# Kernel optimization log

Hardware: AMD Instinct MI355X
Metric: run time of the kernel (lower is better)

## Reference

```python
import jax, jax.numpy as jnp
import numpy as np

N = 50000        # nodes
E = 1600000      # edges (before self loops)
IN = 256         # in_channels
C = 32           # hidden_channels (per head)
H = 4            # heads
OUT = 64         # out_channels
NEG_SLOPE = 0.2  # PyG GATConv default


def setup_inputs() -> dict:
    key = jax.random.key(0)
    ks = jax.random.split(key, 8)
    x = jax.random.normal(ks[0], (N, IN), dtype=jnp.float32)
    edge_index = jax.random.randint(ks[1], (2, E), 0, N, dtype=jnp.int64)
    s = 0.05
    W = jax.random.normal(ks[2], (IN, H * C), dtype=jnp.float32) * s
    att_src = jax.random.normal(ks[3], (H, C), dtype=jnp.float32) * s
    att_dst = jax.random.normal(ks[4], (H, C), dtype=jnp.float32) * s
    bias = jnp.zeros((H * C,), dtype=jnp.float32)
    lin_W = jax.random.normal(ks[5], (H * C, OUT), dtype=jnp.float32) * s
    lin_b = jnp.zeros((OUT,), dtype=jnp.float32)
    return {"x": x, "edge_index": edge_index, "W": W, "att_src": att_src,
            "att_dst": att_dst, "bias": bias, "lin_W": lin_W, "lin_b": lin_b}


def reference(x, edge_index, W, att_src, att_dst, bias, lin_W, lin_b):
    # Linear transform per head: [N, H, C]
    h = (x @ W).reshape(N, H, C)
    # Per-node attention halves (PyG GATConv): [N, H]
    a_src = jnp.einsum('nhc,hc->nh', h, att_src)
    a_dst = jnp.einsum('nhc,hc->nh', h, att_dst)
    # Add self loops (PyG default add_self_loops=True)
    loop = jnp.arange(N, dtype=edge_index.dtype)
    src = jnp.concatenate([edge_index[0], loop])  # message source j
    dst = jnp.concatenate([edge_index[1], loop])  # message target i
    # Edge attention logits: LeakyReLU(a_src[j] + a_dst[i])  -> [E+N, H]
    e = jax.nn.leaky_relu(a_src[src] + a_dst[dst], negative_slope=NEG_SLOPE)
    # Segment softmax over incoming edges of each destination node
    emax = jax.lax.stop_gradient(jax.ops.segment_max(e, dst, num_segments=N))
    emax = jnp.where(jnp.isfinite(emax), emax, 0.0)
    ex = jnp.exp(e - emax[dst])
    denom = jax.ops.segment_sum(ex, dst, num_segments=N)
    alpha = ex / denom[dst]  # [E+N, H]; self loops guarantee denom > 0
    # Weighted scatter-sum of source features: [N, H, C]
    msg = alpha[:, :, None] * h[src]
    agg = jax.ops.segment_sum(msg, dst, num_segments=N)
    out = agg.reshape(N, H * C) + bias  # concat heads + bias
    out = jax.nn.elu(out)
    return out @ lin_W + lin_b
```

## Files before the change

### kernel.cpp

```cpp
#include <hip/hip_runtime.h>
#include <cstdint>
#include <cstddef>

#define N_NODES 50000
#define N_EDGES 1600000
#define TOT_E   (N_EDGES + N_NODES)
#define IN_DIM  256
#define HC      128
#define NHEAD   4
#define OUT_DIM 64

#define SHIFT   7
#define BSZ     128
#define NBUK    ((N_NODES + BSZ - 1) / BSZ)
#define CHUNK   2048
#define EPT     8
#define NCHUNK  ((TOT_E + CHUNK - 1) / CHUNK)
#define NREP    8
#define CAPR    768
#define CAP     (NREP * CAPR)
#define STRIDE  88
#define ROWW    (STRIDE / 2)

#define K1_ROWS 32
#define XPAD 264
#define HPAD 132
#define K1_NB ((N_NODES + K1_ROWS - 1) / K1_ROWS)

#define W2_GEMM_BLK ((HC * IN_DIM) / 256)
#define W2_LIN_BLK  ((OUT_DIM * HC) / 256)

typedef __attribute__((ext_vector_type(8))) short bf16x8;
typedef __attribute__((ext_vector_type(4))) float f32x4;
typedef __attribute__((ext_vector_type(4))) unsigned short u16x4;

static __device__ __forceinline__ uint16_t f2bf(float f) {
    uint32_t u = __float_as_uint(f);
    uint32_t r = (u + 0x7fffu + ((u >> 16) & 1u)) >> 16;
    return (uint16_t)r;
}
static __device__ __forceinline__ float bf_lo(uint32_t u) {
    return __uint_as_float(u << 16);
}
static __device__ __forceinline__ float bf_hi(uint32_t u) {
    return __uint_as_float(u & 0xffff0000u);
}

__global__ __launch_bounds__(256) void w2bf(const float* __restrict__ W,
                                            const float* __restrict__ linW,
                                            uint16_t* __restrict__ wt,
                                            uint16_t* __restrict__ lwt,
                                            int* __restrict__ gcur) {
    if (blockIdx.x < W2_GEMM_BLK) {
        int idx = blockIdx.x * 256 + threadIdx.x;
        int n = idx >> 8, k = idx & 255;
        wt[idx] = f2bf(W[(size_t)k * HC + n]);
        if (idx < NBUK * NREP) gcur[idx] = 0;
    } else {
        int idx = (blockIdx.x - W2_GEMM_BLK) * 256 + threadIdx.x;
        int n = idx >> 7, k = idx & 127;
        float w = linW[(size_t)k * OUT_DIM + n];
        uint16_t h = f2bf(w);
        float hf = __uint_as_float((uint32_t)h << 16);
        lwt[idx] = h;
        lwt[OUT_DIM * HC + idx] = f2bf(w - hf);
    }
}

__global__ __launch_bounds__(256) void k1p3(const float* __restrict__ x,
                                            const uint16_t* __restrict__ wt,
                                            const float* __restrict__ att_src,
                                            const float* __restrict__ att_dst,
                                            uint16_t* __restrict__ hb,
                                            float* __restrict__ a_src,
                                            float* __restrict__ a_dst,
                                            const int* __restrict__ ei,
                                            int* __restrict__ gcur,
                                            uint32_t* __restrict__ binned) {
    __shared__ char smem[K1_ROWS * 528];
    __shared__ float att_s[HC], att_d[HC];
    const int tid = threadIdx.x;

    if (blockIdx.x < K1_NB) {
        uint16_t* xs = (uint16_t*)smem;
        float*    hs = (float*)smem;
        const int wave = tid >> 6;
        const int lane = tid & 63;
        const int m    = lane & 15;
        const int q    = lane >> 4;
        const int row0 = blockIdx.x * K1_ROWS;
        const int wr   = (wave >> 1) * 16;
        const int wc   = (wave & 1) * 64;

        if (tid < HC) { att_s[tid] = att_src[tid]; att_d[tid] = att_dst[tid]; }

        for (int i = tid * 4; i < K1_ROWS * IN_DIM; i += 1024) {
            int r = i >> 8, c = i & 255;
            int gr = row0 + r;
            float4 v = make_float4(0.f, 0.f, 0.f, 0.f);
            if (gr < N_NODES) v = *(const float4*)(x + (size_t)gr * IN_DIM + c);
            uint32_t lo = (uint32_t)f2bf(v.x) | ((uint32_t)f2bf(v.y) << 16);
            uint32_t hi = (uint32_t)f2bf(v.z) | ((uint32_t)f2bf(v.w) << 16);
            *(uint2*)(xs + r * XPAD + c) = make_uint2(lo, hi);
        }
        __syncthreads();

        f32x4 acc[4];
        #pragma unroll
        for (int t = 0; t < 4; ++t) acc[t] = (f32x4){0.f, 0.f, 0.f, 0.f};

        const int arow = wr + m;
        #pragma unroll
        for (int ks = 0; ks < IN_DIM; ks += 32) {
            bf16x8 a = *(const bf16x8*)(xs + arow * XPAD + ks + q * 8);
            #pragma unroll
            for (int t = 0; t < 4; ++t) {
                bf16x8 b = *(const bf16x8*)(wt + (size_t)(wc + t * 16 + m) * IN_DIM + ks + q * 8);
                acc[t] = __builtin_amdgcn_mfma_f32_16x16x32_bf16(a, b, acc[t], 0, 0, 0);
            }
        }
        __syncthreads();

        #pragma unroll
        for (int t = 0; t < 4; ++t)
            #pragma unroll
            for (int r = 0; r < 4; ++r)
                hs[(wr + q * 4 + r) * HPAD + wc + t * 16 + m] = acc[t][r];
        __syncthreads();

        for (int i = tid * 4; i < K1_ROWS * HC; i += 1024) {
            int r = i >> 7, c = i & 127;
            if (row0 + r < N_NODES) {
                float4 v = *(const float4*)(hs + r * HPAD + c);
                uint32_t lo = (uint32_t)f2bf(v.x) | ((uint32_t)f2bf(v.y) << 16);
                uint32_t hi = (uint32_t)f2bf(v.z) | ((uint32_t)f2bf(v.w) << 16);
                *(uint2*)(hb + (size_t)(row0 + r) * HC + c) = make_uint2(lo, hi);
            }
        }
        if (tid < K1_ROWS * NHEAD) {
            int r = tid >> 2, hd = tid & 3;
            if (row0 + r < N_NODES) {
                float s = 0.f, d = 0.f;
                #pragma unroll
                for (int j = 0; j < 32; ++j) {
                    float v = hs[r * HPAD + hd * 32 + j];
                    s = fmaf(v, att_s[hd * 32 + j], s);
                    d = fmaf(v, att_d[hd * 32 + j], d);
                }
                a_src[(row0 + r) * NHEAD + hd] = s;
                a_dst[(row0 + r) * NHEAD + hd] = d;
            }
        }
    } else {
        int* hist = (int*)smem;
        int* lcur = hist + NBUK;
        for (int i = tid; i < NBUK; i += 256) hist[i] = 0;
        __syncthreads();

        uint32_t wreg[EPT];
        const int pblk = blockIdx.x - K1_NB;
        const int rep  = pblk & (NREP - 1);
        const int base = pblk * CHUNK;
        #pragma unroll
        for (int k = 0; k < EPT; ++k) {
            int e = base + k * 256 + tid;
            uint32_t word = 0xFFFFFFFFu;
            if (e < TOT_E) {
                int src, dst;
                if (e < N_EDGES) { src = ei[e]; dst = ei[N_EDGES + e]; }
                else             { src = e - N_EDGES; dst = src; }
                int b = dst >> SHIFT;
                word = (uint32_t)src | ((uint32_t)(dst & (BSZ - 1)) << 16)
                     | ((uint32_t)b << 23);
                atomicAdd(&hist[b], 1);
            }
            wreg[k] = word;
        }
        __syncthreads();
        for (int i = tid; i < NBUK; i += 256) {
            int c = hist[i];
            lcur[i] = c ? atomicAdd(&gcur[rep * NBUK + i], c) : 0;
        }
        __syncthreads();
        #pragma unroll
        for (int k = 0; k < EPT; ++k) {
            uint32_t word = wreg[k];
            if (word != 0xFFFFFFFFu) {
                int b = (int)(word >> 23);
                int pos = atomicAdd(&lcur[b], 1);
                if (pos < CAPR)
                    binned[(size_t)b * CAP + rep * CAPR + pos] = word;
            }
        }
    }
}

__global__ __launch_bounds__(256) void rgrp(const uint32_t* __restrict__ binned,
                                            const int* __restrict__ gcur,
                                            uint16_t* __restrict__ csr,
                                            int* __restrict__ cnt) {
    __shared__ uint32_t lcsr32[BSZ * ROWW];
    __shared__ int ncnt[BSZ];
    const int b   = blockIdx.x;
    const int tid = threadIdx.x;

    for (int j = tid; j < BSZ * ROWW; j += 256) lcsr32[j] = 0;
    if (tid < BSZ) ncnt[tid] = 0;
    __syncthreads();

    uint16_t* lcsr16 = (uint16_t*)lcsr32;
    #pragma unroll
    for (int rep = 0; rep < NREP; ++rep) {
        int c = gcur[rep * NBUK + b];
        if (c > CAPR) c = CAPR;
        const uint32_t* bb = binned + (size_t)b * CAP + rep * CAPR;
        for (int i = tid; i < c; i += 256) {
            uint32_t w = bb[i];
            int dl  = (w >> 16) & (BSZ - 1);
            int pos = atomicAdd(&ncnt[dl], 1);
            if (pos < STRIDE) lcsr16[dl * STRIDE + pos] = (uint16_t)(w & 0xFFFFu);
        }
    }
    __syncthreads();

    const int node0 = b * BSZ;
    uint32_t* csr32 = (uint32_t*)csr;
    for (int j = tid; j < BSZ * ROWW; j += 256) {
        int r = j / ROWW, w = j - r * ROWW;
        int node = node0 + r;
        if (node < N_NODES)
            csr32[(size_t)node * ROWW + w] = lcsr32[j];
    }
    if (tid < BSZ && node0 + tid < N_NODES) cnt[node0 + tid] = ncnt[tid];
}

__global__ __launch_bounds__(512, 6) void q4k7(const uint16_t* __restrict__ csr,
                                               const int* __restrict__ cnt,
                                               const uint32_t* __restrict__ hb32,
                                               const float* __restrict__ a_src,
                                               const float* __restrict__ a_dst,
                                               const float* __restrict__ bias,
                                               const uint16_t* __restrict__ lwt,
                                               const float* __restrict__ linb,
                                               float* __restrict__ out) {
    __shared__ uint16_t as_[32][136];
    const int tid  = threadIdx.x;
    const int wave = tid >> 6;
    const int lane = tid & 63;
    const int g    = lane >> 4;
    const int sl   = lane & 15;
    const int head = sl >> 2;
    const int baseln = g << 4;
    const char*  hb8 = (const char*)hb32 + sl * 16;
    const float* ash = a_src + head;
    const float4 bA = *(const float4*)(bias + sl * 8);
    const float4 bB = *(const float4*)(bias + sl * 8 + 4);

    const int ln   = wave * 4 + g;
    const int node = blockIdx.x * 32 + ln;
    int myc = 0;
    if (node < N_NODES) myc = min(cnt[node], STRIDE);
    const uint16_t* crow = csr + (size_t)min(node, N_NODES - 1) * STRIDE;

    int m1   = max(myc, __shfl_xor(myc, 16, 64));
    int maxc = max(m1,  __shfl_xor(m1, 32, 64));
    const int nit = (maxc + 3) >> 2;
    const float ad = a_dst[min(node, N_NODES - 1) * NHEAD + head];

    uint2 svq = *(const uint2*)(crow + sl * 4);
    const int svlo = (int)svq.x, svhi = (int)svq.y;

    float l = 0.f;
    float acc[8];
    #pragma unroll
    for (int j = 0; j < 8; ++j) acc[j] = 0.f;

    uint4 ph0 = make_uint4(0, 0, 0, 0), ph1 = ph0, ph2 = ph0, ph3 = ph0;
    float pa0 = 0.f, pa1 = 0.f, pa2 = 0.f, pa3 = 0.f;
    if (nit > 0) {
        uint32_t lo = (uint32_t)__shfl(svlo, baseln, 64);
        uint32_t hi = (uint32_t)__shfl(svhi, baseln, 64);
        int s0 = (int)(lo & 0xFFFFu), s1 = (int)(lo >> 16);
        int s2 = (int)(hi & 0xFFFFu), s3 = (int)(hi >> 16);
        pa0 = ash[s0 * NHEAD];
        pa1 = ash[s1 * NHEAD];
        pa2 = ash[s2 * NHEAD];
        pa3 = ash[s3 * NHEAD];
        ph0 = *(const uint4*)(hb8 + ((uint32_t)s0 << 8));
        ph1 = *(const uint4*)(hb8 + ((uint32_t)s1 << 8));
        ph2 = *(const uint4*)(hb8 + ((uint32_t)s2 << 8));
        ph3 = *(const uint4*)(hb8 + ((uint32_t)s3 << 8));
    }

    for (int it = 0; it < nit; ++it) {
        const int i = it * 4;
        const uint4 h0 = ph0, h1 = ph1, h2 = ph2, h3 = ph3;
        const float as0 = pa0, as1 = pa1, as2 = pa2, as3 = pa3;
        if (it + 1 < nit) {
            int s0, s1, s2, s3;
            if (it + 1 < 16) {
                uint32_t lo = (uint32_t)__shfl(svlo, baseln + it + 1, 64);
                uint32_t hi = (uint32_t)__shfl(svhi, baseln + it + 1, 64);
                s0 = (int)(lo & 0xFFFFu); s1 = (int)(lo >> 16);
                s2 = (int)(hi & 0xFFFFu); s3 = (int)(hi >> 16);
            } else {
                u16x4 nv = *(const u16x4*)(crow + i + 4);
                s0 = nv[0]; s1 = nv[1]; s2 = nv[2]; s3 = nv[3];
            }
            pa0 = ash[s0 * NHEAD];
            pa1 = ash[s1 * NHEAD];
            pa2 = ash[s2 * NHEAD];
            pa3 = ash[s3 * NHEAD];
            ph0 = *(const uint4*)(hb8 + ((uint32_t)s0 << 8));
            ph1 = *(const uint4*)(hb8 + ((uint32_t)s1 << 8));
            ph2 = *(const uint4*)(hb8 + ((uint32_t)s2 << 8));
            ph3 = *(const uint4*)(hb8 + ((uint32_t)s3 << 8));
        }

        float e0 = as0 + ad, e1 = as1 + ad, e2 = as2 + ad, e3 = as3 + ad;
        e0 = fmaxf(e0, 0.2f * e0);
        e1 = fmaxf(e1, 0.2f * e1);
        e2 = fmaxf(e2, 0.2f * e2);
        e3 = fmaxf(e3, 0.2f * e3);
        float w0 = __expf(e0), w1 = __expf(e1);
        float w2 = __expf(e2), w3 = __expf(e3);
        w0 = (i + 0 < myc) ? w0 : 0.f;
        w1 = (i + 1 < myc) ? w1 : 0.f;
        w2 = (i + 2 < myc) ? w2 : 0.f;
        w3 = (i + 3 < myc) ? w3 : 0.f;
        l += (w0 + w1) + (w2 + w3);
        acc[0] = fmaf(w0, bf_lo(h0.x), acc[0]); acc[0] = fmaf(w1, bf_lo(h1.x), acc[0]);
        acc[0] = fmaf(w2, bf_lo(h2.x), acc[0]); acc[0] = fmaf(w3, bf_lo(h3.x), acc[0]);
        acc[1] = fmaf(w0, bf_hi(h0.x), acc[1]); acc[1] = fmaf(w1, bf_hi(h1.x), acc[1]);
        acc[1] = fmaf(w2, bf_hi(h2.x), acc[1]); acc[1] = fmaf(w3, bf_hi(h3.x), acc[1]);
        acc[2] = fmaf(w0, bf_lo(h0.y), acc[2]); acc[2] = fmaf(w1, bf_lo(h1.y), acc[2]);
        acc[2] = fmaf(w2, bf_lo(h2.y), acc[2]); acc[2] = fmaf(w3, bf_lo(h3.y), acc[2]);
        acc[3] = fmaf(w0, bf_hi(h0.y), acc[3]); acc[3] = fmaf(w1, bf_hi(h1.y), acc[3]);
        acc[3] = fmaf(w2, bf_hi(h2.y), acc[3]); acc[3] = fmaf(w3, bf_hi(h3.y), acc[3]);
        acc[4] = fmaf(w0, bf_lo(h0.z), acc[4]); acc[4] = fmaf(w1, bf_lo(h1.z), acc[4]);
        acc[4] = fmaf(w2, bf_lo(h2.z), acc[4]); acc[4] = fmaf(w3, bf_lo(h3.z), acc[4]);
        acc[5] = fmaf(w0, bf_hi(h0.z), acc[5]); acc[5] = fmaf(w1, bf_hi(h1.z), acc[5]);
        acc[5] = fmaf(w2, bf_hi(h2.z), acc[5]); acc[5] = fmaf(w3, bf_hi(h3.z), acc[5]);
        acc[6] = fmaf(w0, bf_lo(h0.w), acc[6]); acc[6] = fmaf(w1, bf_lo(h1.w), acc[6]);
        acc[6] = fmaf(w2, bf_lo(h2.w), acc[6]); acc[6] = fmaf(w3, bf_lo(h3.w), acc[6]);
        acc[7] = fmaf(w0, bf_hi(h0.w), acc[7]); acc[7] = fmaf(w1, bf_hi(h1.w), acc[7]);
        acc[7] = fmaf(w2, bf_hi(h2.w), acc[7]); acc[7] = fmaf(w3, bf_hi(h3.w), acc[7]);
    }

    uint4 pk = make_uint4(0, 0, 0, 0);
    if (node < N_NODES) {
        const float inv = 1.f / l;
        float o[8];
        o[0] = fmaf(acc[0], inv, bA.x); o[1] = fmaf(acc[1], inv, bA.y);
        o[2] = fmaf(acc[2], inv, bA.z); o[3] = fmaf(acc[3], inv, bA.w);
        o[4] = fmaf(acc[4], inv, bB.x); o[5] = fmaf(acc[5], inv, bB.y);
        o[6] = fmaf(acc[6], inv, bB.z); o[7] = fmaf(acc[7], inv, bB.w);
        #pragma unroll
        for (int j = 0; j < 8; ++j)
            o[j] = (o[j] > 0.f) ? o[j] : (__expf(o[j]) - 1.f);
        pk.x = (uint32_t)f2bf(o[0]) | ((uint32_t)f2bf(o[1]) << 16);
        pk.y = (uint32_t)f2bf(o[2]) | ((uint32_t)f2bf(o[3]) << 16);
        pk.z = (uint32_t)f2bf(o[4]) | ((uint32_t)f2bf(o[5]) << 16);
        pk.w = (uint32_t)f2bf(o[6]) | ((uint32_t)f2bf(o[7]) << 16);
    }
    *(uint4*)(&as_[ln][sl * 8]) = pk;
    __syncthreads();

    const int m   = lane & 15;
    const int q   = lane >> 4;
    const int wr  = (wave >> 2) * 16;
    const int wcl = (wave & 3) * 16;
    const uint16_t* lwlo = lwt + OUT_DIM * HC;

    f32x4 oacc = (f32x4){0.f, 0.f, 0.f, 0.f};
    const int arow = wr + m;
    #pragma unroll
    for (int ks = 0; ks < HC; ks += 32) {
        bf16x8 a = *(const bf16x8*)(&as_[arow][ks + q * 8]);
        bf16x8 bh = *(const bf16x8*)(lwt  + (size_t)(wcl + m) * HC + ks + q * 8);
        bf16x8 bl = *(const bf16x8*)(lwlo + (size_t)(wcl + m) * HC + ks + q * 8);
        oacc = __builtin_amdgcn_mfma_f32_16x16x32_bf16(a, bh, oacc, 0, 0, 0);
        oacc = __builtin_amdgcn_mfma_f32_16x16x32_bf16(a, bl, oacc, 0, 0, 0);
    }

    const int col  = wcl + m;
    const float lb = linb[col];
    const int grow = blockIdx.x * 32 + wr + q * 4;
    #pragma unroll
    for (int r = 0; r < 4; ++r)
        if (grow + r < N_NODES)
            out[(size_t)(grow + r) * OUT_DIM + col] = oacc[r] + lb;
}

extern "C" void kernel_launch(void* const* d_in, const int* in_sizes, int n_in,
                              void* d_out, int out_size, void* d_ws, size_t ws_size,
                              hipStream_t stream) {
    (void)in_sizes; (void)n_in; (void)out_size; (void)ws_size;
    const float* x       = (const float*)d_in[0];
    const int*   ei      = (const int*)d_in[1];
    const float* W       = (const float*)d_in[2];
    const float* att_src = (const float*)d_in[3];
    const float* att_dst = (const float*)d_in[4];
    const float* bias    = (const float*)d_in[5];
    const float* linW    = (const float*)d_in[6];
    const float* linb    = (const float*)d_in[7];
    float*       out     = (float*)d_out;

    char*  ws  = (char*)d_ws;
    size_t off = 0;
    auto alloc = [&](size_t bytes) -> void* {
        void* p = ws + off;
        off += (bytes + 255) & ~(size_t)255;
        return p;
    };
    uint16_t* hb     = (uint16_t*)alloc((size_t)N_NODES * HC * 2);
    uint16_t* wt     = (uint16_t*)alloc((size_t)HC * IN_DIM * 2);
    float*    a_src  = (float*)alloc((size_t)N_NODES * NHEAD * 4);
    float*    a_dst  = (float*)alloc((size_t)N_NODES * NHEAD * 4);
    int*      gcur   = (int*)alloc((size_t)NBUK * NREP * 4);
    uint32_t* binned = (uint32_t*)alloc((size_t)NBUK * CAP * 4);
    int*      cnt    = (int*)alloc((size_t)N_NODES * 4);
    uint16_t* csr    = (uint16_t*)alloc((size_t)N_NODES * STRIDE * 2);
    uint16_t* lwt    = (uint16_t*)alloc((size_t)2 * OUT_DIM * HC * 2);

    w2bf<<<W2_GEMM_BLK + W2_LIN_BLK, 256, 0, stream>>>(W, linW, wt, lwt, gcur);
    k1p3<<<K1_NB + NCHUNK, 256, 0, stream>>>(x, wt, att_src, att_dst,
                                             hb, a_src, a_dst,
                                             ei, gcur, binned);
    rgrp<<<NBUK, 256, 0, stream>>>(binned, gcur, csr, cnt);
    q4k7<<<(N_NODES + 31) / 32, 512, 0, stream>>>(csr, cnt, (const uint32_t*)hb,
                                                  a_src, a_dst, bias,
                                                  lwt, linb, out);
}
```

Before: 214.8 us.

## Merge all four kernels into one cooperative persistent kernel with grid syncs

Replaces the four separate launches (weight conversion, GEMM plus binning, regrouping, aggregation plus output linear) with one cooperative persistent kernel. The phases are separated by grid-wide syncs and each phase loops over work units with a grid stride. The goal is to remove launch gaps and kernel-boundary drains. Block size grows to 512 and GEMM tiles grow to 64 rows. In exchange, occupancy is capped at the cooperative limit, the larger shared-memory footprint may cut blocks per CU, and the grid barriers add their own cost. The hardcoded 256 CUs also assumes a particular device.

```diff
diff --git a/kernel.cpp b/kernel.cpp
--- a/kernel.cpp
+++ b/kernel.cpp
@@ -1,6 +1,9 @@
 #include <hip/hip_runtime.h>
+#include <hip/hip_cooperative_groups.h>
 #include <cstdint>
 #include <cstddef>
+
+namespace cg = cooperative_groups;
 
 #define N_NODES 50000
 #define N_EDGES 1600000
@@ -14,21 +17,20 @@
 #define BSZ     128
 #define NBUK    ((N_NODES + BSZ - 1) / BSZ)
 #define CHUNK   2048
-#define EPT     8
-#define NCHUNK  ((TOT_E + CHUNK - 1) / CHUNK)
+#define EPT4    4
 #define NREP    8
 #define CAPR    768
 #define CAP     (NREP * CAPR)
 #define STRIDE  88
 #define ROWW    (STRIDE / 2)
 
-#define K1_ROWS 32
 #define XPAD 264
 #define HPAD 132
-#define K1_NB ((N_NODES + K1_ROWS - 1) / K1_ROWS)
-
-#define W2_GEMM_BLK ((HC * IN_DIM) / 256)
-#define W2_LIN_BLK  ((OUT_DIM * HC) / 256)
+
+#define K1U   ((N_NODES + 63) / 64)
+#define P3U   ((TOT_E + CHUNK - 1) / CHUNK)
+#define P1U   (K1U + P3U)
+#define Q4U   ((N_NODES + 31) / 32)
 
 typedef __attribute__((ext_vector_type(8))) short bf16x8;
 typedef __attribute__((ext_vector_type(4))) float f32x4;
@@ -46,350 +48,337 @@
     return __uint_as_float(u & 0xffff0000u);
 }
 
-__global__ __launch_bounds__(256) void w2bf(const float* __restrict__ W,
-                                            const float* __restrict__ linW,
-                                            uint16_t* __restrict__ wt,
-                                            uint16_t* __restrict__ lwt,
-                                            int* __restrict__ gcur) {
-    if (blockIdx.x < W2_GEMM_BLK) {
-        int idx = blockIdx.x * 256 + threadIdx.x;
+__global__ __launch_bounds__(512) void mega(
+        const float* x, const int* ei, const float* W, const float* linW,
+        const float* att_src, const float* att_dst, const float* bias,
+        const float* linb, float* out,
+        uint16_t* wt, uint16_t* lwt, uint16_t* hb,
+        float* a_src, float* a_dst, int* gcur, uint32_t* binned,
+        int* cnt, uint16_t* csr) {
+    cg::grid_group gg = cg::this_grid();
+    __shared__ char smem[64 * 528];
+    __shared__ float att_s[HC], att_d[HC];
+    const int tid  = threadIdx.x;
+    const int gtid = blockIdx.x * 512 + tid;
+    const int gstr = gridDim.x * 512;
+
+    if (tid < HC) { att_s[tid] = att_src[tid]; att_d[tid] = att_dst[tid]; }
+
+    for (int idx = gtid; idx < HC * IN_DIM; idx += gstr) {
         int n = idx >> 8, k = idx & 255;
         wt[idx] = f2bf(W[(size_t)k * HC + n]);
-        if (idx < NBUK * NREP) gcur[idx] = 0;
-    } else {
-        int idx = (blockIdx.x - W2_GEMM_BLK) * 256 + threadIdx.x;
-        int n = idx >> 7, k = idx & 127;
+    }
+    for (int j = gtid; j < OUT_DIM * HC; j += gstr) {
+        int n = j >> 7, k = j & 127;
         float w = linW[(size_t)k * OUT_DIM + n];
         uint16_t h = f2bf(w);
-        float hf = __uint_as_float((uint32_t)h << 16);
-        lwt[idx] = h;
-        lwt[OUT_DIM * HC + idx] = f2bf(w - hf);
-    }
-}
-
-__global__ __launch_bounds__(256) void k1p3(const float* __restrict__ x,
-                                            const uint16_t* __restrict__ wt,
-                                            const float* __restrict__ att_src,
-                                            const float* __restrict__ att_dst,
-                                            uint16_t* __restrict__ hb,
-                                            float* __restrict__ a_src,
-                                            float* __restrict__ a_dst,
-                                            const int* __restrict__ ei,
-                                            int* __restrict__ gcur,
-                                            uint32_t* __restrict__ binned) {
-    __shared__ char smem[K1_ROWS * 528];
-    __shared__ float att_s[HC], att_d[HC];
-    const int tid = threadIdx.x;
-
-    if (blockIdx.x < K1_NB) {
-        uint16_t* xs = (uint16_t*)smem;
-        float*    hs = (float*)smem;
+        lwt[j] = h;
+        lwt[OUT_DIM * HC + j] = f2bf(w - __uint_as_float((uint32_t)h << 16));
+    }
+    for (int i = gtid; i < NBUK * NREP; i += gstr) gcur[i] = 0;
+    gg.sync();
+
+    for (int u = blockIdx.x; u < P1U; u += gridDim.x) {
+        if (u < K1U) {
+            uint16_t* xs = (uint16_t*)smem;
+            float*    hs = (float*)smem;
+            const int wave = tid >> 6;
+            const int lane = tid & 63;
+            const int m    = lane & 15;
+            const int q    = lane >> 4;
+            const int row0 = u * 64;
+            const int wr   = (wave >> 1) * 16;
+            const int wc   = (wave & 1) * 64;
+
+            for (int i = tid * 4; i < 64 * IN_DIM; i += 2048) {
+                int r = i >> 8, c = i & 255;
+                int gr = row0 + r;
+                float4 v = make_float4(0.f, 0.f, 0.f, 0.f);
+                if (gr < N_NODES) v = *(const float4*)(x + (size_t)gr * IN_DIM + c);
+                uint32_t lo = (uint32_t)f2bf(v.x) | ((uint32_t)f2bf(v.y) << 16);
+                uint32_t hi = (uint32_t)f2bf(v.z) | ((uint32_t)f2bf(v.w) << 16);
+                *(uint2*)(xs + r * XPAD + c) = make_uint2(lo, hi);
+            }
+            __syncthreads();
+
+            f32x4 acc[4];
+            #pragma unroll
+            for (int t = 0; t < 4; ++t) acc[t] = (f32x4){0.f, 0.f, 0.f, 0.f};
+            const int arow = wr + m;
+            #pragma unroll
+            for (int ks = 0; ks < IN_DIM; ks += 32) {
+                bf16x8 a = *(const bf16x8*)(xs + arow * XPAD + ks + q * 8);
+                #pragma unroll
+                for (int t = 0; t < 4; ++t) {
+                    bf16x8 b = *(const bf16x8*)(wt + (size_t)(wc + t * 16 + m) * IN_DIM + ks + q * 8);
+                    acc[t] = __builtin_amdgcn_mfma_f32_16x16x32_bf16(a, b, acc[t], 0, 0, 0);
+                }
+            }
+            __syncthreads();
+
+            #pragma unroll
+            for (int t = 0; t < 4; ++t)
+                #pragma unroll
+                for (int r = 0; r < 4; ++r)
+                    hs[(wr + q * 4 + r) * HPAD + wc + t * 16 + m] = acc[t][r];
+            __syncthreads();
+
+            for (int i = tid * 4; i < 64 * HC; i += 2048) {
+                int r = i >> 7, c = i & 127;
+                if (row0 + r < N_NODES) {
+                    float4 v = *(const float4*)(hs + r * HPAD + c);
+                    uint32_t lo = (uint32_t)f2bf(v.x) | ((uint32_t)f2bf(v.y) << 16);
+                    uint32_t hi = (uint32_t)f2bf(v.z) | ((uint32_t)f2bf(v.w) << 16);
+                    *(uint2*)(hb + (size_t)(row0 + r) * HC + c) = make_uint2(lo, hi);
+                }
+            }
+            if (tid < 64 * NHEAD) {
+                int r = tid >> 2, hd = tid & 3;
+                if (row0 + r < N_NODES) {
+                    float s = 0.f, d = 0.f;
+                    #pragma unroll
+                    for (int j = 0; j < 32; ++j) {
+                        float v = hs[r * HPAD + hd * 32 + j];
+                        s = fmaf(v, att_s[hd * 32 + j], s);
+                        d = fmaf(v, att_d[hd * 32 + j], d);
+                    }
+                    a_src[(row0 + r) * NHEAD + hd] = s;
+                    a_dst[(row0 + r) * NHEAD + hd] = d;
+                }
+            }
+        } else {
+            int* hist = (int*)smem;
+            int* lcur = hist + NBUK;
+            for (int i = tid; i < NBUK; i += 512) hist[i] = 0;
+            __syncthreads();
+
+            uint32_t wreg[EPT4];
+            const int pblk = u - K1U;
+            const int rep  = pblk & (NREP - 1);
+            const int base = pblk * CHUNK;
+            #pragma unroll
+            for (int k = 0; k < EPT4; ++k) {
+                int e = base + k * 512 + tid;
+                uint32_t word = 0xFFFFFFFFu;
+                if (e < TOT_E) {
+                    int src, dst;
+                    if (e < N_EDGES) { src = ei[e]; dst = ei[N_EDGES + e]; }
+                    else             { src = e - N_EDGES; dst = src; }
+                    int b = dst >> SHIFT;
+                    word = (uint32_t)src | ((uint32_t)(dst & (BSZ - 1)) << 16)
+                         | ((uint32_t)b << 23);
+                    atomicAdd(&hist[b], 1);
+                }
+                wreg[k] = word;
+            }
+            __syncthreads();
+            for (int i = tid; i < NBUK; i += 512) {
+                int c = hist[i];
+                lcur[i] = c ? atomicAdd(&gcur[rep * NBUK + i], c) : 0;
+            }
+            __syncthreads();
+            #pragma unroll
+            for (int k = 0; k < EPT4; ++k) {
+                uint32_t word = wreg[k];
+                if (word != 0xFFFFFFFFu) {
+                    int b = (int)(word >> 23);
+                    int pos = atomicAdd(&lcur[b], 1);
+                    if (pos < CAPR)
+                        binned[(size_t)b * CAP + rep * CAPR + pos] = word;
+                }
+            }
+        }
+        __syncthreads();
+    }
+    gg.sync();
+
+    {
+        uint32_t* lcsr32 = (uint32_t*)smem;
+        int*      ncnt   = (int*)(smem + BSZ * ROWW * 4);
+        uint16_t* lcsr16 = (uint16_t*)lcsr32;
+        uint32_t* csr32g = (uint32_t*)csr;
+        for (int u = blockIdx.x; u < NBUK; u += gridDim.x) {
+            for (int j = tid; j < BSZ * ROWW; j += 512) lcsr32[j] = 0;
+            if (tid < BSZ) ncnt[tid] = 0;
+            __syncthreads();
+
+            #pragma unroll
+            for (int rep = 0; rep < NREP; ++rep) {
+                int c = gcur[rep * NBUK + u];
+                if (c > CAPR) c = CAPR;
+                const uint32_t* bb = binned + (size_t)u * CAP + rep * CAPR;
+                for (int i = tid; i < c; i += 512) {
+                    uint32_t w = bb[i];
+                    int dl  = (w >> 16) & (BSZ - 1);
+                    int pos = atomicAdd(&ncnt[dl], 1);
+                    if (pos < STRIDE) lcsr16[dl * STRIDE + pos] = (uint16_t)(w & 0xFFFFu);
+                }
+            }
+            __syncthreads();
+
+            const int node0 = u * BSZ;
+            for (int j = tid; j < BSZ * ROWW; j += 512) {
+                int r = j / ROWW, w = j - r * ROWW;
+                if (node0 + r < N_NODES)
+                    csr32g[(size_t)(node0 + r) * ROWW + w] = lcsr32[j];
+            }
+            if (tid < BSZ && node0 + tid < N_NODES) cnt[node0 + tid] = ncnt[tid];
+            __syncthreads();
+        }
+    }
+    gg.sync();
+
+    {
+        uint16_t (*as_)[136] = (uint16_t (*)[136])smem;
         const int wave = tid >> 6;
         const int lane = tid & 63;
-        const int m    = lane & 15;
-        const int q    = lane >> 4;
-        const int row0 = blockIdx.x * K1_ROWS;
-        const int wr   = (wave >> 1) * 16;
-        const int wc   = (wave & 1) * 64;
-
-        if (tid < HC) { att_s[tid] = att_src[tid]; att_d[tid] = att_dst[tid]; }
-
-        for (int i = tid * 4; i < K1_ROWS * IN_DIM; i += 1024) {
-            int r = i >> 8, c = i & 255;
-            int gr = row0 + r;
-            float4 v = make_float4(0.f, 0.f, 0.f, 0.f);
-            if (gr < N_NODES) v = *(const float4*)(x + (size_t)gr * IN_DIM + c);
-            uint32_t lo = (uint32_t)f2bf(v.x) | ((uint32_t)f2bf(v.y) << 16);
-            uint32_t hi = (uint32_t)f2bf(v.z) | ((uint32_t)f2bf(v.w) << 16);
-            *(uint2*)(xs + r * XPAD + c) = make_uint2(lo, hi);
+        const int g    = lane >> 4;
+        const int sl   = lane & 15;
+        const int head = sl >> 2;
+        const int baseln = g << 4;
+        const char*  hb8 = (const char*)hb + sl * 16;
+        const float* ash = a_src + head;
+        const float4 bA = *(const float4*)(bias + sl * 8);
+        const float4 bB = *(const float4*)(bias + sl * 8 + 4);
+        const uint16_t* lwlo = lwt + OUT_DIM * HC;
+
+        for (int u = blockIdx.x; u < Q4U; u += gridDim.x) {
+            const int ln   = wave * 4 + g;
+            const int node = u * 32 + ln;
+            int myc = 0;
+            if (node < N_NODES) myc = min(cnt[node], STRIDE);
+            const uint16_t* crow = csr + (size_t)min(node, N_NODES - 1) * STRIDE;
+
+            int m1   = max(myc, __shfl_xor(myc, 16, 64));
+            int maxc = max(m1,  __shfl_xor(m1, 32, 64));
+            const int nit = (maxc + 3) >> 2;
+            const float ad = a_dst[min(node, N_NODES - 1) * NHEAD + head];
+
+            uint2 svq = *(const uint2*)(crow + sl * 4);
+            const int svlo = (int)svq.x, svhi = (int)svq.y;
+
+            float l = 0.f;
+            float acc[8];
+            #pragma unroll
+            for (int j = 0; j < 8; ++j) acc[j] = 0.f;
+
+            uint4 ph0 = make_uint4(0, 0, 0, 0), ph1 = ph0, ph2 = ph0, ph3 = ph0;
+            float pa0 = 0.f, pa1 = 0.f, pa2 = 0.f, pa3 = 0.f;
+            if (nit > 0) {
+                uint32_t lo = (uint32_t)__shfl(svlo, baseln, 64);
+                uint32_t hi = (uint32_t)__shfl(svhi, baseln, 64);
+                int s0 = (int)(lo & 0xFFFFu), s1 = (int)(lo >> 16);
+                int s2 = (int)(hi & 0xFFFFu), s3 = (int)(hi >> 16);
+                pa0 = ash[s0 * NHEAD];
+                pa1 = ash[s1 * NHEAD];
+                pa2 = ash[s2 * NHEAD];
+                pa3 = ash[s3 * NHEAD];
+                ph0 = *(const uint4*)(hb8 + ((uint32_t)s0 << 8));
+                ph1 = *(const uint4*)(hb8 + ((uint32_t)s1 << 8));
+                ph2 = *(const uint4*)(hb8 + ((uint32_t)s2 << 8));
+                ph3 = *(const uint4*)(hb8 + ((uint32_t)s3 << 8));
+            }
+
+            for (int it = 0; it < nit; ++it) {
+                const int i = it * 4;
+                const uint4 h0 = ph0, h1 = ph1, h2 = ph2, h3 = ph3;
+                const float as0 = pa0, as1 = pa1, as2 = pa2, as3 = pa3;
+                if (it + 1 < nit) {
+                    int s0, s1, s2, s3;
+                    if (it + 1 < 16) {
+                        uint32_t lo = (uint32_t)__shfl(svlo, baseln + it + 1, 64);
+                        uint32_t hi = (uint32_t)__shfl(svhi, baseln + it + 1, 64);
+                        s0 = (int)(lo & 0xFFFFu); s1 = (int)(lo >> 16);
+                        s2 = (int)(hi & 0xFFFFu); s3 = (int)(hi >> 16);
+                    } else {
+                        u16x4 nv = *(const u16x4*)(crow + i + 4);
+                        s0 = nv[0]; s1 = nv[1]; s2 = nv[2]; s3 = nv[3];
+                    }
+                    pa0 = ash[s0 * NHEAD];
+                    pa1 = ash[s1 * NHEAD];
+                    pa2 = ash[s2 * NHEAD];
+                    pa3 = ash[s3 * NHEAD];
+                    ph0 = *(const uint4*)(hb8 + ((uint32_t)s0 << 8));
+                    ph1 = *(const uint4*)(hb8 + ((uint32_t)s1 << 8));
+                    ph2 = *(const uint4*)(hb8 + ((uint32_t)s2 << 8));
+                    ph3 = *(const uint4*)(hb8 + ((uint32_t)s3 << 8));
+                }
+
+                float e0 = as0 + ad, e1 = as1 + ad, e2 = as2 + ad, e3 = as3 + ad;
+                e0 = fmaxf(e0, 0.2f * e0);
+                e1 = fmaxf(e1, 0.2f * e1);
+                e2 = fmaxf(e2, 0.2f * e2);
+                e3 = fmaxf(e3, 0.2f * e3);
+                float w0 = __expf(e0), w1 = __expf(e1);
+                float w2 = __expf(e2), w3 = __expf(e3);
+                w0 = (i + 0 < myc) ? w0 : 0.f;
+                w1 = (i + 1 < myc) ? w1 : 0.f;
+                w2 = (i + 2 < myc) ? w2 : 0.f;
+                w3 = (i + 3 < myc) ? w3 : 0.f;
+                l += (w0 + w1) + (w2 + w3);
+                acc[0] = fmaf(w0, bf_lo(h0.x), acc[0]); acc[0] = fmaf(w1, bf_lo(h1.x), acc[0]);
+                acc[0] = fmaf(w2, bf_lo(h2.x), acc[0]); acc[0] = fmaf(w3, bf_lo(h3.x), acc[0]);
+                acc[1] = fmaf(w0, bf_hi(h0.x), acc[1]); acc[1] = fmaf(w1, bf_hi(h1.x), acc[1]);
+                acc[1] = fmaf(w2, bf_hi(h2.x), acc[1]); acc[1] = fmaf(w3, bf_hi(h3.x), acc[1]);
+                acc[2] = fmaf(w0, bf_lo(h0.y), acc[2]); acc[2] = fmaf(w1, bf_lo(h1.y), acc[2]);
+                acc[2] = fmaf(w2, bf_lo(h2.y), acc[2]); acc[2] = fmaf(w3, bf_lo(h3.y), acc[2]);
+                acc[3] = fmaf(w0, bf_hi(h0.y), acc[3]); acc[3] = fmaf(w1, bf_hi(h1.y), acc[3]);
+                acc[3] = fmaf(w2, bf_hi(h2.y), acc[3]); acc[3] = fmaf(w3, bf_hi(h3.y), acc[3]);
+                acc[4] = fmaf(w0, bf_lo(h0.z), acc[4]); acc[4] = fmaf(w1, bf_lo(h1.z), acc[4]);
+                acc[4] = fmaf(w2, bf_lo(h2.z), acc[4]); acc[4] = fmaf(w3, bf_lo(h3.z), acc[4]);
+                acc[5] = fmaf(w0, bf_hi(h0.z), acc[5]); acc[5] = fmaf(w1, bf_hi(h1.z), acc[5]);
+                acc[5] = fmaf(w2, bf_hi(h2.z), acc[5]); acc[5] = fmaf(w3, bf_hi(h3.z), acc[5]);
+                acc[6] = fmaf(w0, bf_lo(h0.w), acc[6]); acc[6] = fmaf(w1, bf_lo(h1.w), acc[6]);
+                acc[6] = fmaf(w2, bf_lo(h2.w), acc[6]); acc[6] = fmaf(w3, bf_lo(h3.w), acc[6]);
+                acc[7] = fmaf(w0, bf_hi(h0.w), acc[7]); acc[7] = fmaf(w1, bf_hi(h1.w), acc[7]);
+                acc[7] = fmaf(w2, bf_hi(h2.w), acc[7]); acc[7] = fmaf(w3, bf_hi(h3.w), acc[7]);
+            }
+
+            uint4 pk = make_uint4(0, 0, 0, 0);
+            if (node < N_NODES) {
+                const float inv = 1.f / l;
+                float o[8];
+                o[0] = fmaf(acc[0], inv, bA.x); o[1] = fmaf(acc[1], inv, bA.y);
+                o[2] = fmaf(acc[2], inv, bA.z); o[3] = fmaf(acc[3], inv, bA.w);
+                o[4] = fmaf(acc[4], inv, bB.x); o[5] = fmaf(acc[5], inv, bB.y);
+                o[6] = fmaf(acc[6], inv, bB.z); o[7] = fmaf(acc[7], inv, bB.w);
+                #pragma unroll
+                for (int j = 0; j < 8; ++j)
+                    o[j] = (o[j] > 0.f) ? o[j] : (__expf(o[j]) - 1.f);
+                pk.x = (uint32_t)f2bf(o[0]) | ((uint32_t)f2bf(o[1]) << 16);
+                pk.y = (uint32_t)f2bf(o[2]) | ((uint32_t)f2bf(o[3]) << 16);
+                pk.z = (uint32_t)f2bf(o[4]) | ((uint32_t)f2bf(o[5]) << 16);
+                pk.w = (uint32_t)f2bf(o[6]) | ((uint32_t)f2bf(o[7]) << 16);
+            }
+            *(uint4*)(&as_[ln][sl * 8]) = pk;
+            __syncthreads();
+
+            const int m2  = lane & 15;
+            const int q2  = lane >> 4;
+            const int wr2 = (wave >> 2) * 16;
+            const int wcl = (wave & 3) * 16;
+
+            f32x4 oacc = (f32x4){0.f, 0.f, 0.f, 0.f};
+            const int arow = wr2 + m2;
+            #pragma unroll
+            for (int ks = 0; ks < HC; ks += 32) {
+                bf16x8 a  = *(const bf16x8*)(&as_[arow][ks + q2 * 8]);
+                bf16x8 bh = *(const bf16x8*)(lwt  + (size_t)(wcl + m2) * HC + ks + q2 * 8);
+                bf16x8 bl = *(const bf16x8*)(lwlo + (size_t)(wcl + m2) * HC + ks + q2 * 8);
+                oacc = __builtin_amdgcn_mfma_f32_16x16x32_bf16(a, bh, oacc, 0, 0, 0);
+                oacc = __builtin_amdgcn_mfma_f32_16x16x32_bf16(a, bl, oacc, 0, 0, 0);
+            }
+
+            const int col  = wcl + m2;
+            const float lb = linb[col];
+            const int grow = u * 32 + wr2 + q2 * 4;
+            #pragma unroll
+            for (int r = 0; r < 4; ++r)
+                if (grow + r < N_NODES)
+                    out[(size_t)(grow + r) * OUT_DIM + col] = oacc[r] + lb;
+            __syncthreads();
         }
-        __syncthreads();
-
-        f32x4 acc[4];
-        #pragma unroll
-        for (int t = 0; t < 4; ++t) acc[t] = (f32x4){0.f, 0.f, 0.f, 0.f};
-
-        const int arow = wr + m;
-        #pragma unroll
-        for (int ks = 0; ks < IN_DIM; ks += 32) {
-            bf16x8 a = *(const bf16x8*)(xs + arow * XPAD + ks + q * 8);
-            #pragma unroll
-            for (int t = 0; t < 4; ++t) {
-                bf16x8 b = *(const bf16x8*)(wt + (size_t)(wc + t * 16 + m) * IN_DIM + ks + q * 8);
-                acc[t] = __builtin_amdgcn_mfma_f32_16x16x32_bf16(a, b, acc[t], 0, 0, 0);
-            }
-        }
-        __syncthreads();
-
-        #pragma unroll
-        for (int t = 0; t < 4; ++t)
-            #pragma unroll
-            for (int r = 0; r < 4; ++r)
-                hs[(wr + q * 4 + r) * HPAD + wc + t * 16 + m] = acc[t][r];
-        __syncthreads();
-
-        for (int i = tid * 4; i < K1_ROWS * HC; i += 1024) {
-            int r = i >> 7, c = i & 127;
-            if (row0 + r < N_NODES) {
-                float4 v = *(const float4*)(hs + r * HPAD + c);
-                uint32_t lo = (uint32_t)f2bf(v.x) | ((uint32_t)f2bf(v.y) << 16);
-                uint32_t hi = (uint32_t)f2bf(v.z) | ((uint32_t)f2bf(v.w) << 16);
-                *(uint2*)(hb + (size_t)(row0 + r) * HC + c) = make_uint2(lo, hi);
-            }
-        }
-        if (tid < K1_ROWS * NHEAD) {
-            int r = tid >> 2, hd = tid & 3;
-            if (row0 + r < N_NODES) {
-                float s = 0.f, d = 0.f;
-                #pragma unroll
-                for (int j = 0; j < 32; ++j) {
-                    float v = hs[r * HPAD + hd * 32 + j];
-                    s = fmaf(v, att_s[hd * 32 + j], s);
-                    d = fmaf(v, att_d[hd * 32 + j], d);
-                }
-                a_src[(row0 + r) * NHEAD + hd] = s;
-                a_dst[(row0 + r) * NHEAD + hd] = d;
-            }
-        }
-    } else {
-        int* hist = (int*)smem;
-        int* lcur = hist + NBUK;
-        for (int i = tid; i < NBUK; i += 256) hist[i] = 0;
-        __syncthreads();
-
-        uint32_t wreg[EPT];
-        const int pblk = blockIdx.x - K1_NB;
-        const int rep  = pblk & (NREP - 1);
-        const int base = pblk * CHUNK;
-        #pragma unroll
-        for (int k = 0; k < EPT; ++k) {
-            int e = base + k * 256 + tid;
-            uint32_t word = 0xFFFFFFFFu;
-            if (e < TOT_E) {
-                int src, dst;
-                if (e < N_EDGES) { src = ei[e]; dst = ei[N_EDGES + e]; }
-                else             { src = e - N_EDGES; dst = src; }
-                int b = dst >> SHIFT;
-                word = (uint32_t)src | ((uint32_t)(dst & (BSZ - 1)) << 16)
-                     | ((uint32_t)b << 23);
-                atomicAdd(&hist[b], 1);
-            }
-            wreg[k] = word;
-        }
-        __syncthreads();
-        for (int i = tid; i < NBUK; i += 256) {
-            int c = hist[i];
-            lcur[i] = c ? atomicAdd(&gcur[rep * NBUK + i], c) : 0;
-        }
-        __syncthreads();
-        #pragma unroll
-        for (int k = 0; k < EPT; ++k) {
-            uint32_t word = wreg[k];
-            if (word != 0xFFFFFFFFu) {
-                int b = (int)(word >> 23);
-                int pos = atomicAdd(&lcur[b], 1);
-                if (pos < CAPR)
-                    binned[(size_t)b * CAP + rep * CAPR + pos] = word;
-            }
-        }
-    }
-}
-
-__global__ __launch_bounds__(256) void rgrp(const uint32_t* __restrict__ binned,
-                                            const int* __restrict__ gcur,
-                                            uint16_t* __restrict__ csr,
-                                            int* __restrict__ cnt) {
-    __shared__ uint32_t lcsr32[BSZ * ROWW];
-    __shared__ int ncnt[BSZ];
-    const int b   = blockIdx.x;
-    const int tid = threadIdx.x;
-
-    for (int j = tid; j < BSZ * ROWW; j += 256) lcsr32[j] = 0;
-    if (tid < BSZ) ncnt[tid] = 0;
-    __syncthreads();
-
-    uint16_t* lcsr16 = (uint16_t*)lcsr32;
-    #pragma unroll
-    for (int rep = 0; rep < NREP; ++rep) {
-        int c = gcur[rep * NBUK + b];
-        if (c > CAPR) c = CAPR;
-        const uint32_t* bb = binned + (size_t)b * CAP + rep * CAPR;
-        for (int i = tid; i < c; i += 256) {
-            uint32_t w = bb[i];
-            int dl  = (w >> 16) & (BSZ - 1);
-            int pos = atomicAdd(&ncnt[dl], 1);
-            if (pos < STRIDE) lcsr16[dl * STRIDE + pos] = (uint16_t)(w & 0xFFFFu);
-        }
-    }
-    __syncthreads();
-
-    const int node0 = b * BSZ;
-    uint32_t* csr32 = (uint32_t*)csr;
-    for (int j = tid; j < BSZ * ROWW; j += 256) {
-        int r = j / ROWW, w = j - r * ROWW;
-        int node = node0 + r;
-        if (node < N_NODES)
-            csr32[(size_t)node * ROWW + w] = lcsr32[j];
-    }
-    if (tid < BSZ && node0 + tid < N_NODES) cnt[node0 + tid] = ncnt[tid];
-}
-
-__global__ __launch_bounds__(512, 6) void q4k7(const uint16_t* __restrict__ csr,
-                                               const int* __restrict__ cnt,
-                                               const uint32_t* __restrict__ hb32,
-                                               const float* __restrict__ a_src,
-                                               const float* __restrict__ a_dst,
-                                               const float* __restrict__ bias,
-                                               const uint16_t* __restrict__ lwt,
-                                               const float* __restrict__ linb,
-                                               float* __restrict__ out) {
-    __shared__ uint16_t as_[32][136];
-    const int tid  = threadIdx.x;
-    const int wave = tid >> 6;
-    const int lane = tid & 63;
-    const int g    = lane >> 4;
-    const int sl   = lane & 15;
-    const int head = sl >> 2;
-    const int baseln = g << 4;
-    const char*  hb8 = (const char*)hb32 + sl * 16;
-    const float* ash = a_src + head;
-    const float4 bA = *(const float4*)(bias + sl * 8);
-    const float4 bB = *(const float4*)(bias + sl * 8 + 4);
-
-    const int ln   = wave * 4 + g;
-    const int node = blockIdx.x * 32 + ln;
-    int myc = 0;
-    if (node < N_NODES) myc = min(cnt[node], STRIDE);
-    const uint16_t* crow = csr + (size_t)min(node, N_NODES - 1) * STRIDE;
-
-    int m1   = max(myc, __shfl_xor(myc, 16, 64));
-    int maxc = max(m1,  __shfl_xor(m1, 32, 64));
-    const int nit = (maxc + 3) >> 2;
-    const float ad = a_dst[min(node, N_NODES - 1) * NHEAD + head];
-
-    uint2 svq = *(const uint2*)(crow + sl * 4);
-    const int svlo = (int)svq.x, svhi = (int)svq.y;
-
-    float l = 0.f;
-    float acc[8];
-    #pragma unroll
-    for (int j = 0; j < 8; ++j) acc[j] = 0.f;
-
-    uint4 ph0 = make_uint4(0, 0, 0, 0), ph1 = ph0, ph2 = ph0, ph3 = ph0;
-    float pa0 = 0.f, pa1 = 0.f, pa2 = 0.f, pa3 = 0.f;
-    if (nit > 0) {
-        uint32_t lo = (uint32_t)__shfl(svlo, baseln, 64);
-        uint32_t hi = (uint32_t)__shfl(svhi, baseln, 64);
-        int s0 = (int)(lo & 0xFFFFu), s1 = (int)(lo >> 16);
-        int s2 = (int)(hi & 0xFFFFu), s3 = (int)(hi >> 16);
-        pa0 = ash[s0 * NHEAD];
-        pa1 = ash[s1 * NHEAD];
-        pa2 = ash[s2 * NHEAD];
-        pa3 = ash[s3 * NHEAD];
-        ph0 = *(const uint4*)(hb8 + ((uint32_t)s0 << 8));
-        ph1 = *(const uint4*)(hb8 + ((uint32_t)s1 << 8));
-        ph2 = *(const uint4*)(hb8 + ((uint32_t)s2 << 8));
-        ph3 = *(const uint4*)(hb8 + ((uint32_t)s3 << 8));
-    }
-
-    for (int it = 0; it < nit; ++it) {
-        const int i = it * 4;
-        const uint4 h0 = ph0, h1 = ph1, h2 = ph2, h3 = ph3;
-        const float as0 = pa0, as1 = pa1, as2 = pa2, as3 = pa3;
-        if (it + 1 < nit) {
-            int s0, s1, s2, s3;
-            if (it + 1 < 16) {
-                uint32_t lo = (uint32_t)__shfl(svlo, baseln + it + 1, 64);
-                uint32_t hi = (uint32_t)__shfl(svhi, baseln + it + 1, 64);
-                s0 = (int)(lo & 0xFFFFu); s1 = (int)(lo >> 16);
-                s2 = (int)(hi & 0xFFFFu); s3 = (int)(hi >> 16);
-            } else {
-                u16x4 nv = *(const u16x4*)(crow + i + 4);
-                s0 = nv[0]; s1 = nv[1]; s2 = nv[2]; s3 = nv[3];
-            }
-            pa0 = ash[s0 * NHEAD];
-            pa1 = ash[s1 * NHEAD];
-            pa2 = ash[s2 * NHEAD];
-            pa3 = ash[s3 * NHEAD];
-            ph0 = *(const uint4*)(hb8 + ((uint32_t)s0 << 8));
-            ph1 = *(const uint4*)(hb8 + ((uint32_t)s1 << 8));
-            ph2 = *(const uint4*)(hb8 + ((uint32_t)s2 << 8));
-            ph3 = *(const uint4*)(hb8 + ((uint32_t)s3 << 8));
-        }
-
-        float e0 = as0 + ad, e1 = as1 + ad, e2 = as2 + ad, e3 = as3 + ad;
-        e0 = fmaxf(e0, 0.2f * e0);
-        e1 = fmaxf(e1, 0.2f * e1);
-        e2 = fmaxf(e2, 0.2f * e2);
-        e3 = fmaxf(e3, 0.2f * e3);
-        float w0 = __expf(e0), w1 = __expf(e1);
-        float w2 = __expf(e2), w3 = __expf(e3);
-        w0 = (i + 0 < myc) ? w0 : 0.f;
-        w1 = (i + 1 < myc) ? w1 : 0.f;
-        w2 = (i + 2 < myc) ? w2 : 0.f;
-        w3 = (i + 3 < myc) ? w3 : 0.f;
-        l += (w0 + w1) + (w2 + w3);
-        acc[0] = fmaf(w0, bf_lo(h0.x), acc[0]); acc[0] = fmaf(w1, bf_lo(h1.x), acc[0]);
-        acc[0] = fmaf(w2, bf_lo(h2.x), acc[0]); acc[0] = fmaf(w3, bf_lo(h3.x), acc[0]);
-        acc[1] = fmaf(w0, bf_hi(h0.x), acc[1]); acc[1] = fmaf(w1, bf_hi(h1.x), acc[1]);
-        acc[1] = fmaf(w2, bf_hi(h2.x), acc[1]); acc[1] = fmaf(w3, bf_hi(h3.x), acc[1]);
-        acc[2] = fmaf(w0, bf_lo(h0.y), acc[2]); acc[2] = fmaf(w1, bf_lo(h1.y), acc[2]);
-        acc[2] = fmaf(w2, bf_lo(h2.y), acc[2]); acc[2] = fmaf(w3, bf_lo(h3.y), acc[2]);
-        acc[3] = fmaf(w0, bf_hi(h0.y), acc[3]); acc[3] = fmaf(w1, bf_hi(h1.y), acc[3]);
-        acc[3] = fmaf(w2, bf_hi(h2.y), acc[3]); acc[3] = fmaf(w3, bf_hi(h3.y), acc[3]);
-        acc[4] = fmaf(w0, bf_lo(h0.z), acc[4]); acc[4] = fmaf(w1, bf_lo(h1.z), acc[4]);
-        acc[4] = fmaf(w2, bf_lo(h2.z), acc[4]); acc[4] = fmaf(w3, bf_lo(h3.z), acc[4]);
-        acc[5] = fmaf(w0, bf_hi(h0.z), acc[5]); acc[5] = fmaf(w1, bf_hi(h1.z), acc[5]);
-        acc[5] = fmaf(w2, bf_hi(h2.z), acc[5]); acc[5] = fmaf(w3, bf_hi(h3.z), acc[5]);
-        acc[6] = fmaf(w0, bf_lo(h0.w), acc[6]); acc[6] = fmaf(w1, bf_lo(h1.w), acc[6]);
-        acc[6] = fmaf(w2, bf_lo(h2.w), acc[6]); acc[6] = fmaf(w3, bf_lo(h3.w), acc[6]);
-        acc[7] = fmaf(w0, bf_hi(h0.w), acc[7]); acc[7] = fmaf(w1, bf_hi(h1.w), acc[7]);
-        acc[7] = fmaf(w2, bf_hi(h2.w), acc[7]); acc[7] = fmaf(w3, bf_hi(h3.w), acc[7]);
-    }
-
-    uint4 pk = make_uint4(0, 0, 0, 0);
-    if (node < N_NODES) {
-        const float inv = 1.f / l;
-        float o[8];
-        o[0] = fmaf(acc[0], inv, bA.x); o[1] = fmaf(acc[1], inv, bA.y);
-        o[2] = fmaf(acc[2], inv, bA.z); o[3] = fmaf(acc[3], inv, bA.w);
-        o[4] = fmaf(acc[4], inv, bB.x); o[5] = fmaf(acc[5], inv, bB.y);
-        o[6] = fmaf(acc[6], inv, bB.z); o[7] = fmaf(acc[7], inv, bB.w);
-        #pragma unroll
-        for (int j = 0; j < 8; ++j)
-            o[j] = (o[j] > 0.f) ? o[j] : (__expf(o[j]) - 1.f);
-        pk.x = (uint32_t)f2bf(o[0]) | ((uint32_t)f2bf(o[1]) << 16);
-        pk.y = (uint32_t)f2bf(o[2]) | ((uint32_t)f2bf(o[3]) << 16);
-        pk.z = (uint32_t)f2bf(o[4]) | ((uint32_t)f2bf(o[5]) << 16);
-        pk.w = (uint32_t)f2bf(o[6]) | ((uint32_t)f2bf(o[7]) << 16);
-    }
-    *(uint4*)(&as_[ln][sl * 8]) = pk;
-    __syncthreads();
-
-    const int m   = lane & 15;
-    const int q   = lane >> 4;
-    const int wr  = (wave >> 2) * 16;
-    const int wcl = (wave & 3) * 16;
-    const uint16_t* lwlo = lwt + OUT_DIM * HC;
-
-    f32x4 oacc = (f32x4){0.f, 0.f, 0.f, 0.f};
-    const int arow = wr + m;
-    #pragma unroll
-    for (int ks = 0; ks < HC; ks += 32) {
-        bf16x8 a = *(const bf16x8*)(&as_[arow][ks + q * 8]);
-        bf16x8 bh = *(const bf16x8*)(lwt  + (size_t)(wcl + m) * HC + ks + q * 8);
-        bf16x8 bl = *(const bf16x8*)(lwlo + (size_t)(wcl + m) * HC + ks + q * 8);
-        oacc = __builtin_amdgcn_mfma_f32_16x16x32_bf16(a, bh, oacc, 0, 0, 0);
-        oacc = __builtin_amdgcn_mfma_f32_16x16x32_bf16(a, bl, oacc, 0, 0, 0);
-    }
-
-    const int col  = wcl + m;
-    const float lb = linb[col];
-    const int grow = blockIdx.x * 32 + wr + q * 4;
-    #pragma unroll
-    for (int r = 0; r < 4; ++r)
-        if (grow + r < N_NODES)
-            out[(size_t)(grow + r) * OUT_DIM + col] = oacc[r] + lb;
+    }
 }
 
 extern "C" void kernel_launch(void* const* d_in, const int* in_sizes, int n_in,
@@ -423,12 +412,23 @@
     uint16_t* csr    = (uint16_t*)alloc((size_t)N_NODES * STRIDE * 2);
     uint16_t* lwt    = (uint16_t*)alloc((size_t)2 * OUT_DIM * HC * 2);
 
-    w2bf<<<W2_GEMM_BLK + W2_LIN_BLK, 256, 0, stream>>>(W, linW, wt, lwt, gcur);
-    k1p3<<<K1_NB + NCHUNK, 256, 0, stream>>>(x, wt, att_src, att_dst,
-                                             hb, a_src, a_dst,
-                                             ei, gcur, binned);
-    rgrp<<<NBUK, 256, 0, stream>>>(binned, gcur, csr, cnt);
-    q4k7<<<(N_NODES + 31) / 32, 512, 0, stream>>>(csr, cnt, (const uint32_t*)hb,
-                                                  a_src, a_dst, bias,
-                                                  lwt, linb, out);
+    static int maxblk = 0;
+    if (maxblk == 0) {
+        int mb = 0;
+        if (hipOccupancyMaxActiveBlocksPerMultiprocessor(
+                &mb, reinterpret_cast<const void*>(mega), 512, 0) != hipSuccess || mb < 1)
+            mb = 2;
+        maxblk = mb;
+    }
+    int grid = maxblk * 256;
+    if (grid > P1U) grid = P1U;
+
+    void* args[] = { (void*)&x, (void*)&ei, (void*)&W, (void*)&linW,
+                     (void*)&att_src, (void*)&att_dst, (void*)&bias,
+                     (void*)&linb, (void*)&out,
+                     (void*)&wt, (void*)&lwt, (void*)&hb,
+                     (void*)&a_src, (void*)&a_dst, (void*)&gcur,
+                     (void*)&binned, (void*)&cnt, (void*)&csr };
+    hipLaunchCooperativeKernel(reinterpret_cast<const void*>(mega),
+                               dim3(grid), dim3(512), args, 0, stream);
 }
```

Measured after the change: 358.6 us. +66.9%, slower.
